# Kernel tuning notes

Hardware: AMD Instinct MI355X
Metric: run time of the kernel (lower is better)

## Reference

```python
import jax, jax.numpy as jnp
import numpy as np

EYE_PENALTY = 1.0e6


def setup_inputs() -> dict:
    key = jax.random.key(0)
    k1, k2 = jax.random.split(key)
    B, NIN, NK, DK = 512, 1024, 128, 5
    x = jax.random.normal(k1, (B, NIN), dtype=jnp.float32)
    theta = jax.random.normal(k2, (NIN, NK, DK), dtype=jnp.float32) * 0.05
    log_weight_scale = jnp.zeros((NK, DK), dtype=jnp.float32)
    bias = jnp.full((NK,), -1.0, dtype=jnp.float32)
    return {"x": x, "theta": theta, "log_weight_scale": log_weight_scale, "bias": bias}


def reference(x, theta, log_weight_scale, bias):
    # kernel = theta * exp(log_weight_scale) / ||theta||_2 (norm over input dim)
    l2 = jnp.sqrt(jnp.sum(theta * theta, axis=0))            # [K, D]
    kernel = theta * (jnp.exp(log_weight_scale) / l2)[None]   # [NIN, K, D]
    actv = jnp.einsum('bi,ikd->bkd', x, kernel)               # [B, K, D]
    B = x.shape[0]
    # all-pairs L1 distance per kernel: [B, K, B]
    diff = actv[:, :, :, None] - jnp.transpose(actv, (1, 2, 0))[None]  # [B,K,D,B]
    abs_dif = jnp.sum(jnp.abs(diff), axis=2)                  # [B, K, B]
    abs_dif = abs_dif + EYE_PENALTY * jnp.eye(B, dtype=x.dtype)[:, None, :]
    f = jnp.sum(jnp.exp(-abs_dif), axis=2) + bias[None, :]    # [B, K]
    return jnp.concatenate([x, f], axis=1)                    # [B, NIN + K]
```

## Files before the change

kernel.cpp:

```cpp
#include <hip/hip_runtime.h>
#include <math.h>

constexpr int B    = 512;
constexpr int NIN  = 1024;
constexpr int NK   = 128;
constexpr int DK   = 5;
constexpr int NF   = NK * DK;
constexpr int NOUT = NIN + NK;
constexpr int SPLITK = 4;
constexpr int LDA = 88;
#define LOG2E 1.44269504088896f

typedef _Float16 f16x4 __attribute__((ext_vector_type(4)));
typedef _Float16 f16x8 __attribute__((ext_vector_type(8)));
typedef float    f32x4 __attribute__((ext_vector_type(4)));

__global__ __launch_bounds__(256) void gemm_kernel(
        const float* __restrict__ x,
        const float* __restrict__ theta,
        float* __restrict__ actvP,
        float* __restrict__ ps) {
    __shared__ _Float16 Ath[64 * LDA];
    __shared__ _Float16 Bxh[64 * LDA];
    __shared__ float    red2[16][64];

    const int t    = threadIdx.x;
    const int tile = blockIdx.x >> 2;
    const int z    = blockIdx.x & 3;
    const int n0   = (tile >> 3) * 64;
    const int b0   = (tile & 7) * 64;
    const bool do_ps = (tile & 7) == 0;

    const int w   = t >> 6;
    const int l   = t & 63;
    const int r16 = l & 15;
    const int kg  = l >> 4;
    const int tk4 = t >> 4;
    const int tn4 = (t & 15) * 4;

    f32x4 acc0 = {0.f,0.f,0.f,0.f}, acc1 = {0.f,0.f,0.f,0.f};
    f32x4 acc2 = {0.f,0.f,0.f,0.f}, acc3 = {0.f,0.f,0.f,0.f};
    float sq0 = 0.f, sq1 = 0.f, sq2 = 0.f, sq3 = 0.f;

    for (int step = 0; step < 4; ++step) {
        const int kw = z * 256 + step * 64;
        const float4 v0 = *(const float4*)&theta[(kw + tk4*4 + 0)*NF + n0 + tn4];
        const float4 v1 = *(const float4*)&theta[(kw + tk4*4 + 1)*NF + n0 + tn4];
        const float4 v2 = *(const float4*)&theta[(kw + tk4*4 + 2)*NF + n0 + tn4];
        const float4 v3 = *(const float4*)&theta[(kw + tk4*4 + 3)*NF + n0 + tn4];
        if (do_ps) {
            sq0 += v0.x*v0.x + v1.x*v1.x + v2.x*v2.x + v3.x*v3.x;
            sq1 += v0.y*v0.y + v1.y*v1.y + v2.y*v2.y + v3.y*v3.y;
            sq2 += v0.z*v0.z + v1.z*v1.z + v2.z*v2.z + v3.z*v3.z;
            sq3 += v0.w*v0.w + v1.w*v1.w + v2.w*v2.w + v3.w*v3.w;
        }
        {
            f16x4 h;
            h[0]=(_Float16)v0.x; h[1]=(_Float16)v1.x; h[2]=(_Float16)v2.x; h[3]=(_Float16)v3.x;
            *(f16x4*)&Ath[(tn4+0)*LDA + tk4*4] = h;
            h[0]=(_Float16)v0.y; h[1]=(_Float16)v1.y; h[2]=(_Float16)v2.y; h[3]=(_Float16)v3.y;
            *(f16x4*)&Ath[(tn4+1)*LDA + tk4*4] = h;
            h[0]=(_Float16)v0.z; h[1]=(_Float16)v1.z; h[2]=(_Float16)v2.z; h[3]=(_Float16)v3.z;
            *(f16x4*)&Ath[(tn4+2)*LDA + tk4*4] = h;
            h[0]=(_Float16)v0.w; h[1]=(_Float16)v1.w; h[2]=(_Float16)v2.w; h[3]=(_Float16)v3.w;
            *(f16x4*)&Ath[(tn4+3)*LDA + tk4*4] = h;
        }
        #pragma unroll
        for (int i = 0; i < 4; ++i) {
            const int row = i * 16 + tk4;
            const float4 xv = *(const float4*)&x[(b0 + row)*NIN + kw + tn4];
            f16x4 h;
            h[0]=(_Float16)xv.x; h[1]=(_Float16)xv.y;
            h[2]=(_Float16)xv.z; h[3]=(_Float16)xv.w;
            *(f16x4*)&Bxh[row*LDA + tn4] = h;
        }
        __syncthreads();
        #pragma unroll
        for (int half = 0; half < 2; ++half) {
            const f16x8 av  = *(const f16x8*)&Ath[(w*16 + r16)*LDA + kg*8 + half*32];
            const f16x8 bv0 = *(const f16x8*)&Bxh[( 0 + r16)*LDA + kg*8 + half*32];
            const f16x8 bv1 = *(const f16x8*)&Bxh[(16 + r16)*LDA + kg*8 + half*32];
            const f16x8 bv2 = *(const f16x8*)&Bxh[(32 + r16)*LDA + kg*8 + half*32];
            const f16x8 bv3 = *(const f16x8*)&Bxh[(48 + r16)*LDA + kg*8 + half*32];
            acc0 = __builtin_amdgcn_mfma_f32_16x16x32_f16(av, bv0, acc0, 0, 0, 0);
            acc1 = __builtin_amdgcn_mfma_f32_16x16x32_f16(av, bv1, acc1, 0, 0, 0);
            acc2 = __builtin_amdgcn_mfma_f32_16x16x32_f16(av, bv2, acc2, 0, 0, 0);
            acc3 = __builtin_amdgcn_mfma_f32_16x16x32_f16(av, bv3, acc3, 0, 0, 0);
        }
        __syncthreads();
    }
    {
        float* dst = actvP + (size_t)z * NF * B
                   + (size_t)(n0 + w*16 + kg*4) * B + b0 + r16;
        #pragma unroll
        for (int j = 0; j < 4; ++j) {
            dst[j*B +  0] = acc0[j];
            dst[j*B + 16] = acc1[j];
            dst[j*B + 32] = acc2[j];
            dst[j*B + 48] = acc3[j];
        }
    }
    if (do_ps) {
        red2[tk4][tn4+0] = sq0; red2[tk4][tn4+1] = sq1;
        red2[tk4][tn4+2] = sq2; red2[tk4][tn4+3] = sq3;
        __syncthreads();
        if (t < 64) {
            float tot = 0.f;
            #pragma unroll
            for (int rr = 0; rr < 16; ++rr) tot += red2[rr][t];
            ps[z * NF + n0 + t] = tot;
        }
    }
}

__global__ __launch_bounds__(256) void pairwise_kernel(
        const float* __restrict__ actvP,
        const float* __restrict__ ps,
        const float* __restrict__ lws,
        const float* __restrict__ bias,
        const float* __restrict__ x,
        float* __restrict__ out) {
    __shared__ float a[DK * B];
    __shared__ float red[8 * 64];
    __shared__ float s_sh[DK];
    __shared__ float red_ps[DK * SPLITK];

    const int k = blockIdx.x;
    const int e = blockIdx.y;
    const int t = threadIdx.x;

    if (e < 4) {
        const int row = k * 4 + e;
        ((float4*)out)[row * (NOUT/4) + t] = ((const float4*)x)[row * (NIN/4) + t];
    }

    if (t < DK * SPLITK)
        red_ps[t] = ps[(t / DK) * NF + k * DK + (t % DK)];

    float regs[10];
    const float* base = actvP + (size_t)k * DK * B;
    #pragma unroll
    for (int j = 0; j < 10; ++j) {
        const int idx = t + 256 * j;
        float sum = 0.f;
        #pragma unroll
        for (int z = 0; z < SPLITK; ++z) sum += base[(size_t)z * NF * B + idx];
        regs[j] = sum;
    }
    __syncthreads();
    if (t < DK) {
        float sum = 0.f;
        #pragma unroll
        for (int c = 0; c < SPLITK; ++c) sum += red_ps[c * DK + t];
        s_sh[t] = __expf(lws[k * DK + t]) * rsqrtf(sum) * LOG2E;
    }
    __syncthreads();
    #pragma unroll
    for (int j = 0; j < 10; ++j)
        a[t + 256 * j] = regs[j] * s_sh[j >> 1];
    __syncthreads();

    const int g  = t >> 5;
    const int r  = t & 31;
    const int ba = e * 64 + r;
    const int bb = ba + 32;

    const float A0 = a[0*B + ba], A1 = a[1*B + ba], A2 = a[2*B + ba],
                A3 = a[3*B + ba], A4 = a[4*B + ba];
    const float B0 = a[0*B + bb], B1 = a[1*B + bb], B2 = a[2*B + bb],
                B3 = a[3*B + bb], B4 = a[4*B + bb];

    union F4 { float4 v; float f[4]; };

    float accA = 0.f, accB = 0.f;
    const int bp0 = g * 64;
    #pragma unroll 4
    for (int m = 0; m < 16; ++m) {
        const int bp = bp0 + 4 * m;
        F4 w0, w1, w2, w3, w4;
        w0.v = *(const float4*)&a[0*B + bp];
        w1.v = *(const float4*)&a[1*B + bp];
        w2.v = *(const float4*)&a[2*B + bp];
        w3.v = *(const float4*)&a[3*B + bp];
        w4.v = *(const float4*)&a[4*B + bp];
        #pragma unroll
        for (int u = 0; u < 4; ++u) {
            const float dA = ((fabsf(A0 - w0.f[u]) + fabsf(A1 - w1.f[u]))
                            + (fabsf(A2 - w2.f[u]) + fabsf(A3 - w3.f[u])))
                            + fabsf(A4 - w4.f[u]);
            accA += __builtin_amdgcn_exp2f(-dA);
            const float dB = ((fabsf(B0 - w0.f[u]) + fabsf(B1 - w1.f[u]))
                            + (fabsf(B2 - w2.f[u]) + fabsf(B3 - w3.f[u])))
                            + fabsf(B4 - w4.f[u]);
            accB += __builtin_amdgcn_exp2f(-dB);
        }
    }
    red[g * 64 + r]      = accA;
    red[g * 64 + 32 + r] = accB;
    __syncthreads();
    if (t < 64) {
        float f = -1.0f + bias[k];
        #pragma unroll
        for (int gg = 0; gg < 8; ++gg) f += red[gg * 64 + t];
        out[(e * 64 + t) * NOUT + NIN + k] = f;
    }
}

extern "C" void kernel_launch(void* const* d_in, const int* in_sizes, int n_in,
                              void* d_out, int out_size, void* d_ws, size_t ws_size,
                              hipStream_t stream) {
    const float* x     = (const float*)d_in[0];
    const float* theta = (const float*)d_in[1];
    const float* lws   = (const float*)d_in[2];
    const float* bias  = (const float*)d_in[3];
    float* out = (float*)d_out;

    char* wsb = (char*)d_ws;
    float* ps    = (float*)wsb;
    float* actvP = (float*)(wsb + (64 << 10));

    gemm_kernel<<<dim3(320), 256, 0, stream>>>(x, theta, actvP, ps);
    pairwise_kernel<<<dim3(NK, 8), 256, 0, stream>>>(actvP, ps, lws, bias, x, out);
}
```

Before: 27.79 us.

## Compute pairwise L1 distances in packed fp16 with separate reduce-scale kernel

```diff
diff --git a/kernel.cpp b/kernel.cpp
--- a/kernel.cpp
+++ b/kernel.cpp
@@ -1,4 +1,5 @@
 #include <hip/hip_runtime.h>
+#include <hip/hip_fp16.h>
 #include <math.h>
 
 constexpr int B    = 512;
@@ -11,9 +12,12 @@
 constexpr int LDA = 88;
 #define LOG2E 1.44269504088896f
 
+typedef _Float16 f16x2 __attribute__((ext_vector_type(2)));
 typedef _Float16 f16x4 __attribute__((ext_vector_type(4)));
 typedef _Float16 f16x8 __attribute__((ext_vector_type(8)));
 typedef float    f32x4 __attribute__((ext_vector_type(4)));
+
+union H2 { __half2 h; f16x2 v; unsigned u; };
 
 __global__ __launch_bounds__(256) void gemm_kernel(
         const float* __restrict__ x,
@@ -113,17 +117,39 @@
     }
 }
 
-__global__ __launch_bounds__(256) void pairwise_kernel(
+__global__ __launch_bounds__(256) void rs_kernel(
         const float* __restrict__ actvP,
         const float* __restrict__ ps,
         const float* __restrict__ lws,
+        __half* __restrict__ actv16) {
+    const int t   = threadIdx.x;
+    const int row = blockIdx.x * 2 + (t >> 7);
+    const int c4  = (t & 127) * 4;
+
+    const float nrm = ps[0*NF + row] + ps[1*NF + row]
+                    + ps[2*NF + row] + ps[3*NF + row];
+    const float s = __expf(lws[row]) * rsqrtf(nrm) * LOG2E;
+
+    const float* p = actvP + (size_t)row * B + c4;
+    float4 v0 = *(const float4*)(p + 0ull * NF * B);
+    float4 v1 = *(const float4*)(p + 1ull * NF * B);
+    float4 v2 = *(const float4*)(p + 2ull * NF * B);
+    float4 v3 = *(const float4*)(p + 3ull * NF * B);
+    f16x4 h;
+    h[0] = (_Float16)((v0.x + v1.x + v2.x + v3.x) * s);
+    h[1] = (_Float16)((v0.y + v1.y + v2.y + v3.y) * s);
+    h[2] = (_Float16)((v0.z + v1.z + v2.z + v3.z) * s);
+    h[3] = (_Float16)((v0.w + v1.w + v2.w + v3.w) * s);
+    *(f16x4*)&actv16[(size_t)row * B + c4] = h;
+}
+
+__global__ __launch_bounds__(256) void pairwise_kernel(
+        const __half* __restrict__ actv16,
         const float* __restrict__ bias,
         const float* __restrict__ x,
         float* __restrict__ out) {
-    __shared__ float a[DK * B];
-    __shared__ float red[8 * 64];
-    __shared__ float s_sh[DK];
-    __shared__ float red_ps[DK * SPLITK];
+    __shared__ __half a16s[DK * B];
+    __shared__ float  red[8 * 64];
 
     const int k = blockIdx.x;
     const int e = blockIdx.y;
@@ -134,30 +160,11 @@
         ((float4*)out)[row * (NOUT/4) + t] = ((const float4*)x)[row * (NIN/4) + t];
     }
 
-    if (t < DK * SPLITK)
-        red_ps[t] = ps[(t / DK) * NF + k * DK + (t % DK)];
-
-    float regs[10];
-    const float* base = actvP + (size_t)k * DK * B;
-    #pragma unroll
-    for (int j = 0; j < 10; ++j) {
-        const int idx = t + 256 * j;
-        float sum = 0.f;
-        #pragma unroll
-        for (int z = 0; z < SPLITK; ++z) sum += base[(size_t)z * NF * B + idx];
-        regs[j] = sum;
-    }
-    __syncthreads();
-    if (t < DK) {
-        float sum = 0.f;
-        #pragma unroll
-        for (int c = 0; c < SPLITK; ++c) sum += red_ps[c * DK + t];
-        s_sh[t] = __expf(lws[k * DK + t]) * rsqrtf(sum) * LOG2E;
-    }
-    __syncthreads();
-    #pragma unroll
-    for (int j = 0; j < 10; ++j)
-        a[t + 256 * j] = regs[j] * s_sh[j >> 1];
+    {
+        const uint4* src = (const uint4*)(actv16 + (size_t)k * DK * B);
+        ((uint4*)a16s)[t] = src[t];
+        if (t < 64) ((uint4*)a16s)[256 + t] = src[256 + t];
+    }
     __syncthreads();
 
     const int g  = t >> 5;
@@ -165,34 +172,48 @@
     const int ba = e * 64 + r;
     const int bb = ba + 32;
 
-    const float A0 = a[0*B + ba], A1 = a[1*B + ba], A2 = a[2*B + ba],
-                A3 = a[3*B + ba], A4 = a[4*B + ba];
-    const float B0 = a[0*B + bb], B1 = a[1*B + bb], B2 = a[2*B + bb],
-                B3 = a[3*B + bb], B4 = a[4*B + bb];
-
-    union F4 { float4 v; float f[4]; };
+    __half2 A2[DK], B2[DK];
+    #pragma unroll
+    for (int d = 0; d < DK; ++d) {
+        A2[d] = __half2half2(a16s[d * B + ba]);
+        B2[d] = __half2half2(a16s[d * B + bb]);
+    }
+    const H2 ones = {__half2half2(__float2half(1.0f))};
 
     float accA = 0.f, accB = 0.f;
     const int bp0 = g * 64;
-    #pragma unroll 4
-    for (int m = 0; m < 16; ++m) {
-        const int bp = bp0 + 4 * m;
-        F4 w0, w1, w2, w3, w4;
-        w0.v = *(const float4*)&a[0*B + bp];
-        w1.v = *(const float4*)&a[1*B + bp];
-        w2.v = *(const float4*)&a[2*B + bp];
-        w3.v = *(const float4*)&a[3*B + bp];
-        w4.v = *(const float4*)&a[4*B + bp];
-        #pragma unroll
-        for (int u = 0; u < 4; ++u) {
-            const float dA = ((fabsf(A0 - w0.f[u]) + fabsf(A1 - w1.f[u]))
-                            + (fabsf(A2 - w2.f[u]) + fabsf(A3 - w3.f[u])))
-                            + fabsf(A4 - w4.f[u]);
-            accA += __builtin_amdgcn_exp2f(-dA);
-            const float dB = ((fabsf(B0 - w0.f[u]) + fabsf(B1 - w1.f[u]))
-                            + (fabsf(B2 - w2.f[u]) + fabsf(B3 - w3.f[u])))
-                            + fabsf(B4 - w4.f[u]);
-            accB += __builtin_amdgcn_exp2f(-dB);
+
+    union W8 { f16x8 v; __half2 h[4]; };
+    #pragma unroll 2
+    for (int m = 0; m < 8; ++m) {
+        const int bp = bp0 + m * 8;
+        W8 w0, w1, w2, w3, w4;
+        w0.v = *(const f16x8*)&a16s[0*B + bp];
+        w1.v = *(const f16x8*)&a16s[1*B + bp];
+        w2.v = *(const f16x8*)&a16s[2*B + bp];
+        w3.v = *(const f16x8*)&a16s[3*B + bp];
+        w4.v = *(const f16x8*)&a16s[4*B + bp];
+        #pragma unroll
+        for (int c = 0; c < 4; ++c) {
+            __half2 dA = __habs2(__hsub2(A2[0], w0.h[c]));
+            dA = __hadd2(dA, __habs2(__hsub2(A2[1], w1.h[c])));
+            dA = __hadd2(dA, __habs2(__hsub2(A2[2], w2.h[c])));
+            dA = __hadd2(dA, __habs2(__hsub2(A2[3], w3.h[c])));
+            dA = __hadd2(dA, __habs2(__hsub2(A2[4], w4.h[c])));
+            H2 eA; eA.h = h2exp2(__hneg2(dA));
+            __half2 dB = __habs2(__hsub2(B2[0], w0.h[c]));
+            dB = __hadd2(dB, __habs2(__hsub2(B2[1], w1.h[c])));
+            dB = __hadd2(dB, __habs2(__hsub2(B2[2], w2.h[c])));
+            dB = __hadd2(dB, __habs2(__hsub2(B2[3], w3.h[c])));
+            dB = __hadd2(dB, __habs2(__hsub2(B2[4], w4.h[c])));
+            H2 eB; eB.h = h2exp2(__hneg2(dB));
+#if __has_builtin(__builtin_amdgcn_fdot2)
+            accA = __builtin_amdgcn_fdot2(eA.v, ones.v, accA, false);
+            accB = __builtin_amdgcn_fdot2(eB.v, ones.v, accB, false);
+#else
+            accA += __low2float(eA.h) + __high2float(eA.h);
+            accB += __low2float(eB.h) + __high2float(eB.h);
+#endif
         }
     }
     red[g * 64 + r]      = accA;
@@ -216,9 +237,11 @@
     float* out = (float*)d_out;
 
     char* wsb = (char*)d_ws;
-    float* ps    = (float*)wsb;
-    float* actvP = (float*)(wsb + (64 << 10));
+    float*  ps     = (float*)wsb;
+    float*  actvP  = (float*)(wsb + (64 << 10));
+    __half* actv16 = (__half*)(wsb + (64 << 10) + 4 * sizeof(float) * NF * B);
 
     gemm_kernel<<<dim3(320), 256, 0, stream>>>(x, theta, actvP, ps);
-    pairwise_kernel<<<dim3(NK, 8), 256, 0, stream>>>(actvP, ps, lws, bias, x, out);
-}
+    rs_kernel<<<dim3(320), 256, 0, stream>>>(actvP, ps, lws, actv16);
+    pairwise_kernel<<<dim3(NK, 8), 256, 0, stream>>>(actv16, bias, x, out);
+}
```

Result: faster. 27.11 us (-2.4%).
